# Performance work log

Hardware: AMD Instinct MI355X
Metric: run time of the kernel (lower is better)

Reference implementation:

```python
import jax, jax.numpy as jnp
import numpy as np
import math

B, N, H, TDIM, K, R = 32, 4096, 256, 128, 2, 2


def setup_inputs() -> dict:
    key = jax.random.key(0)
    ks = jax.random.split(key, 12)
    s = 1.0 / math.sqrt(H)
    gain = 1.414
    return {
        "x": jax.random.normal(ks[0], (B, N), jnp.float32),
        "t": jax.random.uniform(ks[1], (B,), jnp.float32),
        # scaled so repeated L@x stays O(1) over Chebyshev hops
        "laplacian": jax.random.normal(ks[2], (N, N), jnp.float32) / math.sqrt(N),
        "w_g1": jax.random.normal(ks[3], (1, H, K + 1), jnp.float32) * gain / math.sqrt(1 + H),
        "w_g2": jax.random.normal(ks[4], (H, 1, K + 1), jnp.float32) * gain / math.sqrt(1 + H),
        "w_t1": jax.random.normal(ks[5], (TDIM, H), jnp.float32) / math.sqrt(TDIM),
        "b_t1": jnp.zeros((H,), jnp.float32),
        "w_t2": jax.random.normal(ks[6], (H, H), jnp.float32) * s,
        "b_t2": jnp.zeros((H,), jnp.float32),
        "w_map": jax.random.normal(ks[7], (N, H), jnp.float32) / math.sqrt(N),
        "b_map": jnp.zeros((H,), jnp.float32),
        "res_w": jax.random.normal(ks[8], (R, 3, H, H), jnp.float32) * s,
        "res_b": jnp.zeros((R, 3, H), jnp.float32),
        "w_o1": jax.random.normal(ks[9], (H, H), jnp.float32) * s,
        "b_o1": jnp.zeros((H,), jnp.float32),
        "w_o2": jax.random.normal(ks[10], (H, N), jnp.float32) * s,
        "b_o2": jnp.zeros((N,), jnp.float32),
    }


def timestep_embedding(t, dim, max_period=10000):
    half = dim // 2  # dim is even here
    freqs = jnp.exp(-math.log(max_period) * jnp.arange(half, dtype=t.dtype) / half)
    args = t[:, None] * freqs[None, :]  # [B, half]
    return jnp.concatenate([jnp.cos(args), jnp.sin(args)], axis=-1)  # [B, dim]


def gcn_layer(L, x, w, conv_order):
    xs = [x]
    h = x
    for _ in range(conv_order):
        h = jnp.einsum('mn,bnc->bmc', L, h)  # sparse-style Laplacian propagation (dense here)
        xs.append(h)
    X = jnp.stack(xs, axis=-1)  # [B, N, C, K+1]
    return jnp.einsum('bnik,iok->bno', X, w)


def reference(x, t, laplacian, w_g1, w_g2, w_t1, b_t1, w_t2, b_t2,
              w_map, b_map, res_w, res_b, w_o1, b_o1, w_o2, b_o2):
    silu = jax.nn.silu
    # time embedding path: sinusoidal -> Linear -> SiLU -> Linear
    temb = timestep_embedding(t, TDIM)
    t_out = silu(temb @ w_t1 + b_t1) @ w_t2 + b_t2  # [B, H]
    # GCNBlock: two Chebyshev GCN layers (GCNLayer.forward applies no activation)
    g = gcn_layer(laplacian, x[:, :, None], w_g1, K)  # [B, N, H]
    g = gcn_layer(laplacian, g, w_g2, K)[..., 0]      # [B, N]
    # ResNet_FC on the node signal
    h = g @ w_map + b_map  # [B, H]
    inv_sqrt2 = 1.0 / math.sqrt(2.0)
    for r in range(R):
        z = h
        for i in range(3):
            z = silu(z @ res_w[r, i] + res_b[r, i])
        h = (h + z) * inv_sqrt2
    # output head with time conditioning
    out = silu((h + t_out) @ w_o1 + b_o1) @ w_o2 + b_o2  # [B, N]
    return out
```

## Files before the change

### kernel.cpp

```cpp
#include <hip/hip_runtime.h>
#include <hip/hip_bf16.h>

typedef __bf16 bf16x8 __attribute__((ext_vector_type(8)));
typedef __bf16 bf16x4 __attribute__((ext_vector_type(4)));
typedef float  f32x4  __attribute__((ext_vector_type(4)));


static constexpr size_t WS_A     = 0;
static constexpr size_t WS_TOUT  = 1024;
static constexpr size_t WS_H0    = 65536;
static constexpr size_t WS_UB    = 131072;
static constexpr size_t WS_XB    = 262144;
static constexpr size_t WS_G2B   = 524288;
static constexpr size_t WS_ZB1   = 1048576;
static constexpr size_t WS_ZBSTR = 262144;
static constexpr size_t WS_Z1    = 2097152;
static constexpr size_t WS_ZSTR  = 524288;
static constexpr size_t WS_WMAPT = 4194304;
static constexpr size_t WS_WO2T  = 6291456;
static constexpr size_t WS_LB    = 8388608;

__device__ __forceinline__ f32x4 mfma16(bf16x8 a, bf16x8 b, f32x4 c) {
    return __builtin_amdgcn_mfma_f32_16x16x32_bf16(a, b, c, 0, 0, 0);
}

__device__ __forceinline__ bf16x8 cvt8(const float* p) {
    f32x4 lo = *(const f32x4*)p;
    f32x4 hi = *(const f32x4*)(p + 4);
    bf16x8 r;
    r[0] = (__bf16)lo[0]; r[1] = (__bf16)lo[1]; r[2] = (__bf16)lo[2]; r[3] = (__bf16)lo[3];
    r[4] = (__bf16)hi[0]; r[5] = (__bf16)hi[1]; r[6] = (__bf16)hi[2]; r[7] = (__bf16)hi[3];
    return r;
}

__device__ __forceinline__ float silu_f(float x) { return x / (1.0f + __expf(-x)); }

__device__ __forceinline__ void transpose_tile(const float* __restrict__ src, int sstride,
                                               __bf16* __restrict__ dst, int dstride,
                                               int r0, int c0, float* sh, int tid) {
    const int r = tid >> 3, cg = (tid & 7) * 4;
    f32x4 v = *(const f32x4*)(src + (size_t)(r0 + r) * sstride + c0 + cg);
    sh[r * 33 + cg + 0] = v[0];
    sh[r * 33 + cg + 1] = v[1];
    sh[r * 33 + cg + 2] = v[2];
    sh[r * 33 + cg + 3] = v[3];
    __syncthreads();
    bf16x4 o;
    o[0] = (__bf16)sh[(cg + 0) * 33 + r];
    o[1] = (__bf16)sh[(cg + 1) * 33 + r];
    o[2] = (__bf16)sh[(cg + 2) * 33 + r];
    o[3] = (__bf16)sh[(cg + 3) * 33 + r];
    *(bf16x4*)(dst + (size_t)(c0 + r) * dstride + r0 + cg) = o;
}

__global__ __launch_bounds__(256) void prep_kernel(
    const float* __restrict__ x, const float* __restrict__ t,
    const float* __restrict__ w_g1, const float* __restrict__ w_g2,
    const float* __restrict__ w_t1, const float* __restrict__ b_t1,
    const float* __restrict__ w_t2, const float* __restrict__ b_t2,
    const float* __restrict__ w_map, const float* __restrict__ w_o2,
    char* __restrict__ ws)
{
    __shared__ float sh[1056];
    const int bi = blockIdx.x, tid = threadIdx.x;
    if (bi == 0) {
        const float g10 = w_g1[tid * 3 + 0], g11 = w_g1[tid * 3 + 1], g12 = w_g1[tid * 3 + 2];
        const float g20 = w_g2[tid * 3 + 0], g21 = w_g2[tid * 3 + 1], g22 = w_g2[tid * 3 + 2];
        float p[9] = {g10 * g20, g10 * g21, g10 * g22,
                      g11 * g20, g11 * g21, g11 * g22,
                      g12 * g20, g12 * g21, g12 * g22};
        const int wv = tid >> 6, ln = tid & 63;
#pragma unroll
        for (int j = 0; j < 9; ++j) {
            float v = p[j];
#pragma unroll
            for (int off = 32; off > 0; off >>= 1) v += __shfl_down(v, off);
            if (ln == 0) sh[wv * 9 + j] = v;
        }
        __syncthreads();
        if (tid == 0) {
            float s[9];
#pragma unroll
            for (int j = 0; j < 9; ++j) s[j] = sh[j] + sh[9 + j] + sh[18 + j] + sh[27 + j];
            float* a = (float*)(ws + WS_A);
            a[0] = s[0];
            a[1] = s[1] + s[3];
            a[2] = s[2] + s[4] + s[6];
            a[3] = s[5] + s[7];
            a[4] = s[8];
        }
    } else if (bi < 33) {
        const int b = bi - 1;
        float* t_out = (float*)(ws + WS_TOUT);
        if (tid < 64) {
            float fr = __expf(-9.210340371976184f * (float)tid * (1.0f / 64.0f));
            float ang = t[b] * fr;
            sh[tid]      = __cosf(ang);
            sh[64 + tid] = __sinf(ang);
        }
        __syncthreads();
        float acc = b_t1[tid];
        for (int j = 0; j < 128; ++j) acc += sh[j] * w_t1[j * 256 + tid];
        sh[128 + tid] = silu_f(acc);
        __syncthreads();
        float acc2 = b_t2[tid];
        for (int j = 0; j < 256; ++j) acc2 += sh[128 + j] * w_t2[j * 256 + tid];
        t_out[b * 256 + tid] = acc2;
    } else if (bi < 41) {
        f32x4* p = (f32x4*)(ws + WS_H0);
        f32x4 z = {0.f, 0.f, 0.f, 0.f};
        p[(bi - 33) * 256 + tid] = z;
    } else if (bi < 105) {
        const int e = ((bi - 41) * 256 + tid) * 8;
        *(bf16x8*)((__bf16*)(ws + WS_XB) + e) = cvt8(x + e);
    } else if (bi < 1129) {
        const int ti = bi - 105;
        transpose_tile(w_map, 256, (__bf16*)(ws + WS_WMAPT), 4096,
                       (ti >> 3) * 32, (ti & 7) * 32, sh, tid);
    } else {
        const int ti = bi - 1129;
        transpose_tile(w_o2, 4096, (__bf16*)(ws + WS_WO2T), 256,
                       (ti & 7) * 32, (ti >> 3) * 32, sh, tid);
    }
}

__global__ __launch_bounds__(1024) void hop1_kernel(
    const float* __restrict__ L, const __bf16* __restrict__ xb,
    float* __restrict__ zout, __bf16* __restrict__ zb_out,
    __bf16* __restrict__ Lb)
{
    __shared__ float red[16][16][33];
    const int bi = blockIdx.x, tid = threadIdx.x;
    const int wave = tid >> 6, lane = tid & 63;
    const int l15 = lane & 15, q = lane >> 4;
    const int m0 = bi * 16;
    const int kbase = wave * 256;

    const float*  lp  = L  + (size_t)(m0 + l15) * 4096;
    __bf16*       lbp = Lb + (size_t)(m0 + l15) * 4096;
    const __bf16* b0p = xb + (size_t)l15 * 4096;
    const __bf16* b1p = xb + (size_t)(l15 + 16) * 4096;

    f32x4 acc0 = {0,0,0,0}, acc1 = {0,0,0,0};
#pragma unroll
    for (int ks = 0; ks < 8; ++ks) {
        const int k = kbase + ks * 32 + q * 8;
        bf16x8 a  = cvt8(lp + k);
        *(bf16x8*)(lbp + k) = a;
        bf16x8 b0 = *(const bf16x8*)(b0p + k);
        bf16x8 b1 = *(const bf16x8*)(b1p + k);
        acc0 = mfma16(a, b0, acc0);
        acc1 = mfma16(a, b1, acc1);
    }
#pragma unroll
    for (int r = 0; r < 4; ++r) {
        red[wave][q * 4 + r][l15]      = acc0[r];
        red[wave][q * 4 + r][l15 + 16] = acc1[r];
    }
    __syncthreads();
    if (tid < 512) {
        const int m = tid & 15, b = tid >> 4;
        float v = 0.f;
#pragma unroll
        for (int w = 0; w < 16; ++w) v += red[w][m][b];
        zout[(size_t)b * 4096 + m0 + m] = v;
        zb_out[(size_t)b * 4096 + m0 + m] = (__bf16)v;
    }
}

__global__ __launch_bounds__(1024) void hop_bf_kernel(
    const __bf16* __restrict__ Lb, const __bf16* __restrict__ zb_in,
    float* __restrict__ zout, __bf16* __restrict__ zb_out)
{
    __shared__ float red[16][16][33];
    const int bi = blockIdx.x, tid = threadIdx.x;
    const int wave = tid >> 6, lane = tid & 63;
    const int l15 = lane & 15, q = lane >> 4;
    const int m0 = bi * 16;
    const int kbase = wave * 256;

    const __bf16* ap  = Lb + (size_t)(m0 + l15) * 4096;
    const __bf16* b0p = zb_in + (size_t)l15 * 4096;
    const __bf16* b1p = zb_in + (size_t)(l15 + 16) * 4096;

    f32x4 acc0 = {0,0,0,0}, acc1 = {0,0,0,0};
#pragma unroll
    for (int ks = 0; ks < 8; ++ks) {
        const int k = kbase + ks * 32 + q * 8;
        bf16x8 a  = *(const bf16x8*)(ap + k);
        bf16x8 b0 = *(const bf16x8*)(b0p + k);
        bf16x8 b1 = *(const bf16x8*)(b1p + k);
        acc0 = mfma16(a, b0, acc0);
        acc1 = mfma16(a, b1, acc1);
    }
#pragma unroll
    for (int r = 0; r < 4; ++r) {
        red[wave][q * 4 + r][l15]      = acc0[r];
        red[wave][q * 4 + r][l15 + 16] = acc1[r];
    }
    __syncthreads();
    if (tid < 512) {
        const int m = tid & 15, b = tid >> 4;
        float v = 0.f;
#pragma unroll
        for (int w = 0; w < 16; ++w) v += red[w][m][b];
        zout[(size_t)b * 4096 + m0 + m] = v;
        if (zb_out) zb_out[(size_t)b * 4096 + m0 + m] = (__bf16)v;
    }
}

__global__ __launch_bounds__(256) void combine_kernel(
    const float* __restrict__ x,
    const float* __restrict__ z1, const float* __restrict__ z2,
    const float* __restrict__ z3, const float* __restrict__ z4,
    const float* __restrict__ a, __bf16* __restrict__ g2b)
{
    const int i = blockIdx.x * 256 + threadIdx.x;
    const float a0 = a[0], a1 = a[1], a2 = a[2], a3 = a[3], a4 = a[4];
    f32x4 r = a0 * ((const f32x4*)x)[i] + a1 * ((const f32x4*)z1)[i]
            + a2 * ((const f32x4*)z2)[i] + a3 * ((const f32x4*)z3)[i]
            + a4 * ((const f32x4*)z4)[i];
    bf16x4 o;
    o[0] = (__bf16)r[0]; o[1] = (__bf16)r[1]; o[2] = (__bf16)r[2]; o[3] = (__bf16)r[3];
    ((bf16x4*)g2b)[i] = o;
}

__global__ __launch_bounds__(256) void map_gemm_kernel(
    const __bf16* __restrict__ g2b, const __bf16* __restrict__ w_mapT,
    float* __restrict__ h0)
{
    __shared__ float red[4][16][32];
    const int bi = blockIdx.x, tid = threadIdx.x;
    const int wave = tid >> 6, lane = tid & 63;
    const int l15 = lane & 15, q = lane >> 4;
    const int btile = bi & 1;
    const int hp = (bi >> 1) & 7;
    const int kc = bi >> 4;
    const int kbase = kc * 512 + wave * 128;

    const __bf16* ap  = g2b + (size_t)(btile * 16 + l15) * 4096;
    const __bf16* bp0 = w_mapT + (size_t)(hp * 32 + l15) * 4096;
    const __bf16* bp1 = w_mapT + (size_t)(hp * 32 + 16 + l15) * 4096;

    f32x4 acc0 = {0,0,0,0}, acc1 = {0,0,0,0};
#pragma unroll
    for (int ks = 0; ks < 4; ++ks) {
        const int k = kbase + ks * 32 + q * 8;
        bf16x8 a  = *(const bf16x8*)(ap + k);
        bf16x8 b0 = *(const bf16x8*)(bp0 + k);
        bf16x8 b1 = *(const bf16x8*)(bp1 + k);
        acc0 = mfma16(a, b0, acc0);
        acc1 = mfma16(a, b1, acc1);
    }
#pragma unroll
    for (int r = 0; r < 4; ++r) {
        red[wave][q * 4 + r][l15]      = acc0[r];
        red[wave][q * 4 + r][l15 + 16] = acc1[r];
    }
    __syncthreads();
    const int b_l = tid >> 4, hl = tid & 15;
#pragma unroll
    for (int s = 0; s < 2; ++s) {
        const int h_l = hl + s * 16;
        float v = red[0][b_l][h_l] + red[1][b_l][h_l] + red[2][b_l][h_l] + red[3][b_l][h_l];
        atomicAdd(h0 + (size_t)(btile * 16 + b_l) * 256 + hp * 32 + h_l, v);
    }
}

__global__ __launch_bounds__(1024) void resnet_kernel(
    const float* __restrict__ h0, const float* __restrict__ b_map,
    const float* __restrict__ res_w, const float* __restrict__ res_b,
    const float* __restrict__ t_out, const float* __restrict__ w_o1,
    const float* __restrict__ b_o1, __bf16* __restrict__ u_b)
{
    __shared__ float zs[256];
    __shared__ float part[4][256];
    const int b = blockIdx.x, tid = threadIdx.x;
    const int col = tid & 255, kg = tid >> 8;

    float hv = 0.f;
    if (kg == 0) {
        hv = h0[b * 256 + col] + b_map[col];
        zs[col] = hv;
    }
    __syncthreads();

#pragma unroll
    for (int r = 0; r < 2; ++r) {
        for (int i = 0; i < 3; ++i) {
            const float* W = res_w + ((size_t)(r * 3 + i) << 16) + (size_t)kg * 64 * 256 + col;
            const float* zp = zs + kg * 64;
            float a0 = 0, a1 = 0, a2 = 0, a3 = 0;
#pragma unroll
            for (int j = 0; j < 64; j += 4) {
                a0 += zp[j]     * W[(j)     * 256];
                a1 += zp[j + 1] * W[(j + 1) * 256];
                a2 += zp[j + 2] * W[(j + 2) * 256];
                a3 += zp[j + 3] * W[(j + 3) * 256];
            }
            part[kg][col] = (a0 + a1) + (a2 + a3);
            __syncthreads();
            if (kg == 0) {
                zs[col] = silu_f(res_b[(r * 3 + i) * 256 + col]
                                 + part[0][col] + part[1][col] + part[2][col] + part[3][col]);
            }
            __syncthreads();
        }
        if (kg == 0) {
            hv = (hv + zs[col]) * 0.70710678118654752f;
            zs[col] = hv;
        }
        __syncthreads();
    }

    if (kg == 0) zs[col] = hv + t_out[b * 256 + col];
    __syncthreads();
    {
        const float* W = w_o1 + (size_t)kg * 64 * 256 + col;
        const float* zp = zs + kg * 64;
        float a0 = 0, a1 = 0, a2 = 0, a3 = 0;
#pragma unroll
        for (int j = 0; j < 64; j += 4) {
            a0 += zp[j]     * W[(j)     * 256];
            a1 += zp[j + 1] * W[(j + 1) * 256];
            a2 += zp[j + 2] * W[(j + 2) * 256];
            a3 += zp[j + 3] * W[(j + 3) * 256];
        }
        part[kg][col] = (a0 + a1) + (a2 + a3);
    }
    __syncthreads();
    if (kg == 0) {
        u_b[b * 256 + col] = (__bf16)silu_f(b_o1[col]
            + part[0][col] + part[1][col] + part[2][col] + part[3][col]);
    }
}

__global__ __launch_bounds__(256) void out_gemm_kernel(
    const __bf16* __restrict__ u_b, const __bf16* __restrict__ w_o2T,
    const float* __restrict__ b_o2, float* __restrict__ out)
{
    const int tid = threadIdx.x;
    const int wave = tid >> 6, lane = tid & 63;
    const int l15 = lane & 15, q = lane >> 4;
    const int g = blockIdx.x * 4 + wave;
    const int btile = g & 1;
    const int n0 = (g >> 1) * 32;

    const __bf16* ap  = u_b + (size_t)(btile * 16 + l15) * 256;
    const __bf16* bp0 = w_o2T + (size_t)(n0 + l15) * 256;
    const __bf16* bp1 = w_o2T + (size_t)(n0 + 16 + l15) * 256;

    f32x4 acc0 = {0,0,0,0}, acc1 = {0,0,0,0};
#pragma unroll
    for (int ks = 0; ks < 8; ++ks) {
        const int k = ks * 32 + q * 8;
        bf16x8 a  = *(const bf16x8*)(ap + k);
        bf16x8 b0 = *(const bf16x8*)(bp0 + k);
        bf16x8 b1 = *(const bf16x8*)(bp1 + k);
        acc0 = mfma16(a, b0, acc0);
        acc1 = mfma16(a, b1, acc1);
    }
    const int row = btile * 16 + q * 4;
    const int na = n0 + l15, nb = n0 + 16 + l15;
#pragma unroll
    for (int r = 0; r < 4; ++r) {
        out[(size_t)(row + r) * 4096 + na] = acc0[r] + b_o2[na];
        out[(size_t)(row + r) * 4096 + nb] = acc1[r] + b_o2[nb];
    }
}

extern "C" void kernel_launch(void* const* d_in, const int* in_sizes, int n_in,
                              void* d_out, int out_size, void* d_ws, size_t ws_size,
                              hipStream_t stream)
{
    (void)in_sizes; (void)n_in; (void)out_size; (void)ws_size;
    const float* x     = (const float*)d_in[0];
    const float* t     = (const float*)d_in[1];
    const float* L     = (const float*)d_in[2];
    const float* w_g1  = (const float*)d_in[3];
    const float* w_g2  = (const float*)d_in[4];
    const float* w_t1  = (const float*)d_in[5];
    const float* b_t1  = (const float*)d_in[6];
    const float* w_t2  = (const float*)d_in[7];
    const float* b_t2  = (const float*)d_in[8];
    const float* w_map = (const float*)d_in[9];
    const float* b_map = (const float*)d_in[10];
    const float* res_w = (const float*)d_in[11];
    const float* res_b = (const float*)d_in[12];
    const float* w_o1  = (const float*)d_in[13];
    const float* b_o1  = (const float*)d_in[14];
    const float* w_o2  = (const float*)d_in[15];
    const float* b_o2  = (const float*)d_in[16];
    float* out = (float*)d_out;
    char* ws = (char*)d_ws;

    float*  a_c  = (float*)(ws + WS_A);
    float*  tout = (float*)(ws + WS_TOUT);
    float*  h0   = (float*)(ws + WS_H0);
    __bf16* u_b  = (__bf16*)(ws + WS_UB);
    __bf16* xb   = (__bf16*)(ws + WS_XB);
    __bf16* g2b  = (__bf16*)(ws + WS_G2B);
    __bf16* zb1  = (__bf16*)(ws + WS_ZB1);
    __bf16* zb2  = (__bf16*)(ws + WS_ZB1 + WS_ZBSTR);
    __bf16* zb3  = (__bf16*)(ws + WS_ZB1 + 2 * WS_ZBSTR);
    float*  z1   = (float*)(ws + WS_Z1);
    float*  z2   = (float*)(ws + WS_Z1 + WS_ZSTR);
    float*  z3   = (float*)(ws + WS_Z1 + 2 * WS_ZSTR);
    float*  z4   = (float*)(ws + WS_Z1 + 3 * WS_ZSTR);
    __bf16* w_mapT = (__bf16*)(ws + WS_WMAPT);
    __bf16* w_o2T  = (__bf16*)(ws + WS_WO2T);
    __bf16* Lb     = (__bf16*)(ws + WS_LB);

    prep_kernel<<<2153, 256, 0, stream>>>(x, t, w_g1, w_g2, w_t1, b_t1, w_t2, b_t2,
                                          w_map, w_o2, ws);
    hop1_kernel<<<256, 1024, 0, stream>>>(L, xb, z1, zb1, Lb);
    hop_bf_kernel<<<256, 1024, 0, stream>>>(Lb, zb1, z2, zb2);
    hop_bf_kernel<<<256, 1024, 0, stream>>>(Lb, zb2, z3, zb3);
    hop_bf_kernel<<<256, 1024, 0, stream>>>(Lb, zb3, z4, nullptr);
    combine_kernel<<<128, 256, 0, stream>>>(x, z1, z2, z3, z4, a_c, g2b);
    map_gemm_kernel<<<128, 256, 0, stream>>>(g2b, w_mapT, h0);
    resnet_kernel<<<32, 1024, 0, stream>>>(h0, b_map, res_w, res_b, tout, w_o1, b_o1, u_b);
    out_gemm_kernel<<<64, 256, 0, stream>>>(u_b, w_o2T, b_o2, out);
}
```

Baseline: 229.2 us.

## Fuse combine into last hop and merge map, resnet and output GEMMs into one tail kernel

The final Chebyshev hop kernel now computes the weighted combination of x and the hop results directly, which removes the separate combine kernel and the fourth fp32 hop buffer. The map GEMM, ResNet MLP and output GEMM are merged into one 32-block tail kernel. That kernel uses fp32 FMA reads of the original w_map and w_o2, so the bf16 weight transposes in prep and their atomics go away. The aim is fewer launches and less prep traffic. The cost is that only 32 workgroups each stream the full w_map and w_o2 with scalar loads instead of MFMA, which may leave the tail latency-bound.

Result: slower. 326.1 us (+42.3%).

```diff
diff --git a/kernel.cpp b/kernel.cpp
--- a/kernel.cpp
+++ b/kernel.cpp
@@ -8,16 +8,10 @@
 
 static constexpr size_t WS_A     = 0;
 static constexpr size_t WS_TOUT  = 1024;
-static constexpr size_t WS_H0    = 65536;
-static constexpr size_t WS_UB    = 131072;
 static constexpr size_t WS_XB    = 262144;
-static constexpr size_t WS_G2B   = 524288;
-static constexpr size_t WS_ZB1   = 1048576;
-static constexpr size_t WS_ZBSTR = 262144;
-static constexpr size_t WS_Z1    = 2097152;
-static constexpr size_t WS_ZSTR  = 524288;
-static constexpr size_t WS_WMAPT = 4194304;
-static constexpr size_t WS_WO2T  = 6291456;
+static constexpr size_t WS_G2F   = 524288;
+static constexpr size_t WS_ZB    = 1048576;
+static constexpr size_t WS_ZF    = 2097152;
 static constexpr size_t WS_LB    = 8388608;
 
 __device__ __forceinline__ f32x4 mfma16(bf16x8 a, bf16x8 b, f32x4 c) {
@@ -35,33 +29,14 @@
 
 __device__ __forceinline__ float silu_f(float x) { return x / (1.0f + __expf(-x)); }
 
-__device__ __forceinline__ void transpose_tile(const float* __restrict__ src, int sstride,
-                                               __bf16* __restrict__ dst, int dstride,
-                                               int r0, int c0, float* sh, int tid) {
-    const int r = tid >> 3, cg = (tid & 7) * 4;
-    f32x4 v = *(const f32x4*)(src + (size_t)(r0 + r) * sstride + c0 + cg);
-    sh[r * 33 + cg + 0] = v[0];
-    sh[r * 33 + cg + 1] = v[1];
-    sh[r * 33 + cg + 2] = v[2];
-    sh[r * 33 + cg + 3] = v[3];
-    __syncthreads();
-    bf16x4 o;
-    o[0] = (__bf16)sh[(cg + 0) * 33 + r];
-    o[1] = (__bf16)sh[(cg + 1) * 33 + r];
-    o[2] = (__bf16)sh[(cg + 2) * 33 + r];
-    o[3] = (__bf16)sh[(cg + 3) * 33 + r];
-    *(bf16x4*)(dst + (size_t)(c0 + r) * dstride + r0 + cg) = o;
-}
-
 __global__ __launch_bounds__(256) void prep_kernel(
     const float* __restrict__ x, const float* __restrict__ t,
     const float* __restrict__ w_g1, const float* __restrict__ w_g2,
     const float* __restrict__ w_t1, const float* __restrict__ b_t1,
     const float* __restrict__ w_t2, const float* __restrict__ b_t2,
-    const float* __restrict__ w_map, const float* __restrict__ w_o2,
     char* __restrict__ ws)
 {
-    __shared__ float sh[1056];
+    __shared__ float sh[448];
     const int bi = blockIdx.x, tid = threadIdx.x;
     if (bi == 0) {
         const float g10 = w_g1[tid * 3 + 0], g11 = w_g1[tid * 3 + 1], g12 = w_g1[tid * 3 + 2];
@@ -106,27 +81,15 @@
         float acc2 = b_t2[tid];
         for (int j = 0; j < 256; ++j) acc2 += sh[128 + j] * w_t2[j * 256 + tid];
         t_out[b * 256 + tid] = acc2;
-    } else if (bi < 41) {
-        f32x4* p = (f32x4*)(ws + WS_H0);
-        f32x4 z = {0.f, 0.f, 0.f, 0.f};
-        p[(bi - 33) * 256 + tid] = z;
-    } else if (bi < 105) {
-        const int e = ((bi - 41) * 256 + tid) * 8;
+    } else {
+        const int e = ((bi - 33) * 256 + tid) * 8;
         *(bf16x8*)((__bf16*)(ws + WS_XB) + e) = cvt8(x + e);
-    } else if (bi < 1129) {
-        const int ti = bi - 105;
-        transpose_tile(w_map, 256, (__bf16*)(ws + WS_WMAPT), 4096,
-                       (ti >> 3) * 32, (ti & 7) * 32, sh, tid);
-    } else {
-        const int ti = bi - 1129;
-        transpose_tile(w_o2, 4096, (__bf16*)(ws + WS_WO2T), 256,
-                       (ti & 7) * 32, (ti >> 3) * 32, sh, tid);
     }
 }
 
 __global__ __launch_bounds__(1024) void hop1_kernel(
     const float* __restrict__ L, const __bf16* __restrict__ xb,
-    float* __restrict__ zout, __bf16* __restrict__ zb_out,
+    float* __restrict__ zf_out, __bf16* __restrict__ zb_out,
     __bf16* __restrict__ Lb)
 {
     __shared__ float red[16][16][33];
@@ -163,14 +126,14 @@
         float v = 0.f;
 #pragma unroll
         for (int w = 0; w < 16; ++w) v += red[w][m][b];
-        zout[(size_t)b * 4096 + m0 + m] = v;
+        zf_out[(size_t)b * 4096 + m0 + m] = v;
         zb_out[(size_t)b * 4096 + m0 + m] = (__bf16)v;
     }
 }
 
-__global__ __launch_bounds__(1024) void hop_bf_kernel(
+__global__ __launch_bounds__(1024) void hop_mid_kernel(
     const __bf16* __restrict__ Lb, const __bf16* __restrict__ zb_in,
-    float* __restrict__ zout, __bf16* __restrict__ zb_out)
+    float* __restrict__ zf_out, __bf16* __restrict__ zb_out)
 {
     __shared__ float red[16][16][33];
     const int bi = blockIdx.x, tid = threadIdx.x;
@@ -204,51 +167,36 @@
         float v = 0.f;
 #pragma unroll
         for (int w = 0; w < 16; ++w) v += red[w][m][b];
-        zout[(size_t)b * 4096 + m0 + m] = v;
-        if (zb_out) zb_out[(size_t)b * 4096 + m0 + m] = (__bf16)v;
-    }
-}
-
-__global__ __launch_bounds__(256) void combine_kernel(
+        zf_out[(size_t)b * 4096 + m0 + m] = v;
+        zb_out[(size_t)b * 4096 + m0 + m] = (__bf16)v;
+    }
+}
+
+__global__ __launch_bounds__(1024) void hop4_kernel(
+    const __bf16* __restrict__ Lb, const __bf16* __restrict__ zb_in,
     const float* __restrict__ x,
-    const float* __restrict__ z1, const float* __restrict__ z2,
-    const float* __restrict__ z3, const float* __restrict__ z4,
-    const float* __restrict__ a, __bf16* __restrict__ g2b)
-{
-    const int i = blockIdx.x * 256 + threadIdx.x;
-    const float a0 = a[0], a1 = a[1], a2 = a[2], a3 = a[3], a4 = a[4];
-    f32x4 r = a0 * ((const f32x4*)x)[i] + a1 * ((const f32x4*)z1)[i]
-            + a2 * ((const f32x4*)z2)[i] + a3 * ((const f32x4*)z3)[i]
-            + a4 * ((const f32x4*)z4)[i];
-    bf16x4 o;
-    o[0] = (__bf16)r[0]; o[1] = (__bf16)r[1]; o[2] = (__bf16)r[2]; o[3] = (__bf16)r[3];
-    ((bf16x4*)g2b)[i] = o;
-}
-
-__global__ __launch_bounds__(256) void map_gemm_kernel(
-    const __bf16* __restrict__ g2b, const __bf16* __restrict__ w_mapT,
-    float* __restrict__ h0)
-{
-    __shared__ float red[4][16][32];
+    const float* __restrict__ z1f, const float* __restrict__ z2f,
+    const float* __restrict__ z3f, const float* __restrict__ a_c,
+    float* __restrict__ g2f)
+{
+    __shared__ float red[16][16][33];
     const int bi = blockIdx.x, tid = threadIdx.x;
     const int wave = tid >> 6, lane = tid & 63;
     const int l15 = lane & 15, q = lane >> 4;
-    const int btile = bi & 1;
-    const int hp = (bi >> 1) & 7;
-    const int kc = bi >> 4;
-    const int kbase = kc * 512 + wave * 128;
-
-    const __bf16* ap  = g2b + (size_t)(btile * 16 + l15) * 4096;
-    const __bf16* bp0 = w_mapT + (size_t)(hp * 32 + l15) * 4096;
-    const __bf16* bp1 = w_mapT + (size_t)(hp * 32 + 16 + l15) * 4096;
+    const int m0 = bi * 16;
+    const int kbase = wave * 256;
+
+    const __bf16* ap  = Lb + (size_t)(m0 + l15) * 4096;
+    const __bf16* b0p = zb_in + (size_t)l15 * 4096;
+    const __bf16* b1p = zb_in + (size_t)(l15 + 16) * 4096;
 
     f32x4 acc0 = {0,0,0,0}, acc1 = {0,0,0,0};
 #pragma unroll
-    for (int ks = 0; ks < 4; ++ks) {
+    for (int ks = 0; ks < 8; ++ks) {
         const int k = kbase + ks * 32 + q * 8;
         bf16x8 a  = *(const bf16x8*)(ap + k);
-        bf16x8 b0 = *(const bf16x8*)(bp0 + k);
-        bf16x8 b1 = *(const bf16x8*)(bp1 + k);
+        bf16x8 b0 = *(const bf16x8*)(b0p + k);
+        bf16x8 b1 = *(const bf16x8*)(b1p + k);
         acc0 = mfma16(a, b0, acc0);
         acc1 = mfma16(a, b1, acc1);
     }
@@ -258,65 +206,60 @@
         red[wave][q * 4 + r][l15 + 16] = acc1[r];
     }
     __syncthreads();
-    const int b_l = tid >> 4, hl = tid & 15;
-#pragma unroll
-    for (int s = 0; s < 2; ++s) {
-        const int h_l = hl + s * 16;
-        float v = red[0][b_l][h_l] + red[1][b_l][h_l] + red[2][b_l][h_l] + red[3][b_l][h_l];
-        atomicAdd(h0 + (size_t)(btile * 16 + b_l) * 256 + hp * 32 + h_l, v);
-    }
-}
-
-__global__ __launch_bounds__(1024) void resnet_kernel(
-    const float* __restrict__ h0, const float* __restrict__ b_map,
+    if (tid < 512) {
+        const int m = tid & 15, b = tid >> 4;
+        float v = 0.f;
+#pragma unroll
+        for (int w = 0; w < 16; ++w) v += red[w][m][b];
+        const size_t idx = (size_t)b * 4096 + m0 + m;
+        g2f[idx] = a_c[0] * x[idx] + a_c[1] * z1f[idx] + a_c[2] * z2f[idx]
+                 + a_c[3] * z3f[idx] + a_c[4] * v;
+    }
+}
+
+__global__ __launch_bounds__(1024) void tail_kernel(
+    const float* __restrict__ g2f, const float* __restrict__ w_map,
+    const float* __restrict__ b_map,
     const float* __restrict__ res_w, const float* __restrict__ res_b,
     const float* __restrict__ t_out, const float* __restrict__ w_o1,
-    const float* __restrict__ b_o1, __bf16* __restrict__ u_b)
-{
+    const float* __restrict__ b_o1,
+    const float* __restrict__ w_o2, const float* __restrict__ b_o2,
+    float* __restrict__ out)
+{
+    __shared__ float g2s[4096];
     __shared__ float zs[256];
     __shared__ float part[4][256];
+    __shared__ float us[256];
     const int b = blockIdx.x, tid = threadIdx.x;
     const int col = tid & 255, kg = tid >> 8;
 
+    ((f32x4*)g2s)[tid] = ((const f32x4*)(g2f + (size_t)b * 4096))[tid];
+    __syncthreads();
+
+    {
+        const float* W = w_map + (size_t)(kg * 1024) * 256 + col;
+        const float* zp = g2s + kg * 1024;
+        float a0 = 0, a1 = 0, a2 = 0, a3 = 0;
+#pragma unroll 8
+        for (int j = 0; j < 1024; j += 4) {
+            a0 += zp[j]     * W[(size_t)(j)     * 256];
+            a1 += zp[j + 1] * W[(size_t)(j + 1) * 256];
+            a2 += zp[j + 2] * W[(size_t)(j + 2) * 256];
+            a3 += zp[j + 3] * W[(size_t)(j + 3) * 256];
+        }
+        part[kg][col] = (a0 + a1) + (a2 + a3);
+    }
+    __syncthreads();
     float hv = 0.f;
-    if (kg == 0) {
-        hv = h0[b * 256 + col] + b_map[col];
+    if (tid < 256) {
+        hv = b_map[col] + part[0][col] + part[1][col] + part[2][col] + part[3][col];
         zs[col] = hv;
     }
     __syncthreads();
 
-#pragma unroll
-    for (int r = 0; r < 2; ++r) {
-        for (int i = 0; i < 3; ++i) {
-            const float* W = res_w + ((size_t)(r * 3 + i) << 16) + (size_t)kg * 64 * 256 + col;
-            const float* zp = zs + kg * 64;
-            float a0 = 0, a1 = 0, a2 = 0, a3 = 0;
-#pragma unroll
-            for (int j = 0; j < 64; j += 4) {
-                a0 += zp[j]     * W[(j)     * 256];
-                a1 += zp[j + 1] * W[(j + 1) * 256];
-                a2 += zp[j + 2] * W[(j + 2) * 256];
-                a3 += zp[j + 3] * W[(j + 3) * 256];
-            }
-            part[kg][col] = (a0 + a1) + (a2 + a3);
-            __syncthreads();
-            if (kg == 0) {
-                zs[col] = silu_f(res_b[(r * 3 + i) * 256 + col]
-                                 + part[0][col] + part[1][col] + part[2][col] + part[3][col]);
-            }
-            __syncthreads();
-        }
-        if (kg == 0) {
-            hv = (hv + zs[col]) * 0.70710678118654752f;
-            zs[col] = hv;
-        }
-        __syncthreads();
-    }
-
-    if (kg == 0) zs[col] = hv + t_out[b * 256 + col];
-    __syncthreads();
-    {
-        const float* W = w_o1 + (size_t)kg * 64 * 256 + col;
+    auto layer = [&](const float* __restrict__ Wbase, const float* __restrict__ bias,
+                     float* __restrict__ dst) {
+        const float* W = Wbase + (size_t)kg * 64 * 256 + col;
         const float* zp = zs + kg * 64;
         float a0 = 0, a1 = 0, a2 = 0, a3 = 0;
 #pragma unroll
@@ -327,45 +270,42 @@
             a3 += zp[j + 3] * W[(j + 3) * 256];
         }
         part[kg][col] = (a0 + a1) + (a2 + a3);
-    }
-    __syncthreads();
-    if (kg == 0) {
-        u_b[b * 256 + col] = (__bf16)silu_f(b_o1[col]
-            + part[0][col] + part[1][col] + part[2][col] + part[3][col]);
-    }
-}
-
-__global__ __launch_bounds__(256) void out_gemm_kernel(
-    const __bf16* __restrict__ u_b, const __bf16* __restrict__ w_o2T,
-    const float* __restrict__ b_o2, float* __restrict__ out)
-{
-    const int tid = threadIdx.x;
-    const int wave = tid >> 6, lane = tid & 63;
-    const int l15 = lane & 15, q = lane >> 4;
-    const int g = blockIdx.x * 4 + wave;
-    const int btile = g & 1;
-    const int n0 = (g >> 1) * 32;
-
-    const __bf16* ap  = u_b + (size_t)(btile * 16 + l15) * 256;
-    const __bf16* bp0 = w_o2T + (size_t)(n0 + l15) * 256;
-    const __bf16* bp1 = w_o2T + (size_t)(n0 + 16 + l15) * 256;
-
-    f32x4 acc0 = {0,0,0,0}, acc1 = {0,0,0,0};
-#pragma unroll
-    for (int ks = 0; ks < 8; ++ks) {
-        const int k = ks * 32 + q * 8;
-        bf16x8 a  = *(const bf16x8*)(ap + k);
-        bf16x8 b0 = *(const bf16x8*)(bp0 + k);
-        bf16x8 b1 = *(const bf16x8*)(bp1 + k);
-        acc0 = mfma16(a, b0, acc0);
-        acc1 = mfma16(a, b1, acc1);
-    }
-    const int row = btile * 16 + q * 4;
-    const int na = n0 + l15, nb = n0 + 16 + l15;
-#pragma unroll
-    for (int r = 0; r < 4; ++r) {
-        out[(size_t)(row + r) * 4096 + na] = acc0[r] + b_o2[na];
-        out[(size_t)(row + r) * 4096 + nb] = acc1[r] + b_o2[nb];
+        __syncthreads();
+        if (tid < 256) {
+            dst[col] = silu_f(bias[col]
+                + part[0][col] + part[1][col] + part[2][col] + part[3][col]);
+        }
+        __syncthreads();
+    };
+
+#pragma unroll
+    for (int r = 0; r < 2; ++r) {
+        for (int i = 0; i < 3; ++i)
+            layer(res_w + ((size_t)(r * 3 + i) << 16), res_b + (r * 3 + i) * 256, zs);
+        if (tid < 256) {
+            hv = (hv + zs[col]) * 0.70710678118654752f;
+            zs[col] = hv;
+        }
+        __syncthreads();
+    }
+
+    if (tid < 256) zs[col] = hv + t_out[b * 256 + col];
+    __syncthreads();
+    layer(w_o1, b_o1, us);
+
+#pragma unroll
+    for (int p = 0; p < 4; ++p) {
+        const int n = p * 1024 + tid;
+        float a0 = 0, a1 = 0, a2 = 0, a3 = 0;
+        const float* W = w_o2 + n;
+#pragma unroll 8
+        for (int h = 0; h < 256; h += 4) {
+            a0 += us[h]     * W[(size_t)(h)     * 4096];
+            a1 += us[h + 1] * W[(size_t)(h + 1) * 4096];
+            a2 += us[h + 2] * W[(size_t)(h + 2) * 4096];
+            a3 += us[h + 3] * W[(size_t)(h + 3) * 4096];
+        }
+        out[(size_t)b * 4096 + n] = b_o2[n] + (a0 + a1) + (a2 + a3);
     }
 }
 
@@ -396,29 +336,21 @@
 
     float*  a_c  = (float*)(ws + WS_A);
     float*  tout = (float*)(ws + WS_TOUT);
-    float*  h0   = (float*)(ws + WS_H0);
-    __bf16* u_b  = (__bf16*)(ws + WS_UB);
     __bf16* xb   = (__bf16*)(ws + WS_XB);
-    __bf16* g2b  = (__bf16*)(ws + WS_G2B);
-    __bf16* zb1  = (__bf16*)(ws + WS_ZB1);
-    __bf16* zb2  = (__bf16*)(ws + WS_ZB1 + WS_ZBSTR);
-    __bf16* zb3  = (__bf16*)(ws + WS_ZB1 + 2 * WS_ZBSTR);
-    float*  z1   = (float*)(ws + WS_Z1);
-    float*  z2   = (float*)(ws + WS_Z1 + WS_ZSTR);
-    float*  z3   = (float*)(ws + WS_Z1 + 2 * WS_ZSTR);
-    float*  z4   = (float*)(ws + WS_Z1 + 3 * WS_ZSTR);
-    __bf16* w_mapT = (__bf16*)(ws + WS_WMAPT);
-    __bf16* w_o2T  = (__bf16*)(ws + WS_WO2T);
-    __bf16* Lb     = (__bf16*)(ws + WS_LB);
-
-    prep_kernel<<<2153, 256, 0, stream>>>(x, t, w_g1, w_g2, w_t1, b_t1, w_t2, b_t2,
-                                          w_map, w_o2, ws);
-    hop1_kernel<<<256, 1024, 0, stream>>>(L, xb, z1, zb1, Lb);
-    hop_bf_kernel<<<256, 1024, 0, stream>>>(Lb, zb1, z2, zb2);
-    hop_bf_kernel<<<256, 1024, 0, stream>>>(Lb, zb2, z3, zb3);
-    hop_bf_kernel<<<256, 1024, 0, stream>>>(Lb, zb3, z4, nullptr);
-    combine_kernel<<<128, 256, 0, stream>>>(x, z1, z2, z3, z4, a_c, g2b);
-    map_gemm_kernel<<<128, 256, 0, stream>>>(g2b, w_mapT, h0);
-    resnet_kernel<<<32, 1024, 0, stream>>>(h0, b_map, res_w, res_b, tout, w_o1, b_o1, u_b);
-    out_gemm_kernel<<<64, 256, 0, stream>>>(u_b, w_o2T, b_o2, out);
-}
+    float*  g2f  = (float*)(ws + WS_G2F);
+    __bf16* zb1  = (__bf16*)(ws + WS_ZB);
+    __bf16* zb2  = zb1 + 131072;
+    __bf16* zb3  = zb2 + 131072;
+    float*  z1f  = (float*)(ws + WS_ZF);
+    float*  z2f  = z1f + 131072;
+    float*  z3f  = z2f + 131072;
+    __bf16* Lb   = (__bf16*)(ws + WS_LB);
+
+    prep_kernel<<<97, 256, 0, stream>>>(x, t, w_g1, w_g2, w_t1, b_t1, w_t2, b_t2, ws);
+    hop1_kernel<<<256, 1024, 0, stream>>>(L, xb, z1f, zb1, Lb);
+    hop_mid_kernel<<<256, 1024, 0, stream>>>(Lb, zb1, z2f, zb2);
+    hop_mid_kernel<<<256, 1024, 0, stream>>>(Lb, zb2, z3f, zb3);
+    hop4_kernel<<<256, 1024, 0, stream>>>(Lb, zb3, x, z1f, z2f, z3f, a_c, g2f);
+    tail_kernel<<<32, 1024, 0, stream>>>(g2f, w_map, b_map, res_w, res_b, tout,
+                                         w_o1, b_o1, w_o2, b_o2, out);
+}
```
